# Kernel optimization log

Measured on AMD Instinct MI355X. Metric: run time of the kernel, lower is better.

The kernel has to match this reference:

```python
import jax, jax.numpy as jnp
import numpy as np

B, T, D = 2, 2048, 2048
N_HEADS, N_KV = 16, 4
HD = D // N_HEADS  # 128
ROPE_BASE = 10000.0


def _rope_tables(t, dim, base=ROPE_BASE):
    inv_freq = 1.0 / (base ** (jnp.arange(0, dim, 2, dtype=jnp.float32) / dim))
    freqs = jnp.arange(t, dtype=jnp.float32)[:, None] * inv_freq[None, :]  # (T, dim/2)
    emb = jnp.concatenate([freqs, freqs], axis=-1)  # (T, dim)
    return jnp.cos(emb), jnp.sin(emb)


def _rotate_half(x):
    x1, x2 = jnp.split(x, 2, axis=-1)
    return jnp.concatenate([-x2, x1], axis=-1)


def _apply_rope(x, cos, sin):
    # x: (B, H, T, hd); cos/sin: (T, hd)
    return x * cos[None, None] + _rotate_half(x) * sin[None, None]


def setup_inputs() -> dict:
    key = jax.random.key(0)
    ks = jax.random.split(key, 5)
    s = 0.02
    return {
        "x": jax.random.normal(ks[0], (B, T, D), jnp.float32),
        "wq": jax.random.normal(ks[1], (D, N_HEADS * HD), jnp.float32) * s,
        "wk": jax.random.normal(ks[2], (D, N_KV * HD), jnp.float32) * s,
        "wv": jax.random.normal(ks[3], (D, N_KV * HD), jnp.float32) * s,
        "wo": jax.random.normal(ks[4], (D, D), jnp.float32) * s,
    }


def reference(x, wq, wk, wv, wo):
    b, t, c = x.shape
    n_rep = N_HEADS // N_KV
    scale = 1.0 / np.sqrt(HD)

    q = (x @ wq).reshape(b, t, N_HEADS, HD).transpose(0, 2, 1, 3)  # (B,H,T,hd)
    k = (x @ wk).reshape(b, t, N_KV, HD).transpose(0, 2, 1, 3)     # (B,Hkv,T,hd)
    v = (x @ wv).reshape(b, t, N_KV, HD).transpose(0, 2, 1, 3)

    cos, sin = _rope_tables(t, HD)
    q = _apply_rope(q, cos, sin)
    k = _apply_rope(k, cos, sin)

    # repeat_kv (GQA)
    k = jnp.repeat(k, n_rep, axis=1)  # (B,H,T,hd)
    v = jnp.repeat(v, n_rep, axis=1)

    scores = jnp.einsum("bhqd,bhkd->bhqk", q, k) * scale
    causal = jnp.tril(jnp.ones((t, t), dtype=bool))
    scores = jnp.where(causal[None, None], scores, -jnp.inf)
    attn = jax.nn.softmax(scores, axis=-1)
    out = jnp.einsum("bhqk,bhkd->bhqd", attn, v)
    out = out.transpose(0, 2, 1, 3).reshape(b, t, c)
    return out @ wo
```

## Files before the change

### kernel.cpp

```cpp
#include <hip/hip_runtime.h>
#include <hip/hip_bf16.h>
#include <math.h>

#define B_   2
#define T_   2048
#define D_   2048
#define NH_  16
#define NKV_ 4
#define HD_  128
#define MROWS (B_*T_)
#define NQKV  (NH_*HD_ + 2*NKV_*HD_)

typedef __bf16 bf16_t;
typedef __bf16 bf16x8 __attribute__((ext_vector_type(8)));
typedef __bf16 bf16x4 __attribute__((ext_vector_type(4)));
typedef float  floatx4 __attribute__((ext_vector_type(4)));

__device__ __forceinline__ void async_copy16(const bf16_t* gsrc, bf16_t* ldst) {
  __builtin_amdgcn_global_load_lds(
      (const __attribute__((address_space(1))) unsigned int*)gsrc,
      (__attribute__((address_space(3))) unsigned int*)ldst, 16, 0, 0);
}

__global__ void prep_fused(const float* __restrict__ s0, const float* __restrict__ s1,
                           const float* __restrict__ s2, const float* __restrict__ s3,
                           const float* __restrict__ sx,
                           bf16_t* __restrict__ d0, bf16_t* __restrict__ d1,
                           bf16_t* __restrict__ d2, bf16_t* __restrict__ d3,
                           bf16_t* __restrict__ dx) {
  const int z = blockIdx.z;
  const int tx = threadIdx.x, ty = threadIdx.y;
  if (z == 4) {
    int i = ((blockIdx.y * 64 + blockIdx.x) * 256 + ty * 32 + tx) * 8;
    float4 a = *(const float4*)(sx + i);
    float4 b = *(const float4*)(sx + i + 4);
    bf16x8 v;
    v[0]=(bf16_t)a.x; v[1]=(bf16_t)a.y; v[2]=(bf16_t)a.z; v[3]=(bf16_t)a.w;
    v[4]=(bf16_t)b.x; v[5]=(bf16_t)b.y; v[6]=(bf16_t)b.z; v[7]=(bf16_t)b.w;
    *(bf16x8*)(dx + i) = v;
    return;
  }
  const int N = (z == 1 || z == 2) ? 512 : 2048;
  const int n0 = blockIdx.x * 32;
  if (n0 >= N) return;
  const float* src = (z == 0) ? s0 : (z == 1) ? s1 : (z == 2) ? s2 : s3;
  bf16_t*      dst = (z == 0) ? d0 : (z == 1) ? d1 : (z == 2) ? d2 : d3;
  const int K = 2048;
  __shared__ float tile[32][33];
  int k0 = blockIdx.y * 32;
#pragma unroll
  for (int r = 0; r < 4; r++)
    tile[ty + r*8][tx] = src[(size_t)(k0 + ty + r*8) * N + n0 + tx];
  __syncthreads();
#pragma unroll
  for (int r = 0; r < 4; r++)
    dst[(size_t)(n0 + ty + r*8) * K + k0 + tx] = (bf16_t)tile[tx][ty + r*8];
}

template <typename OUT_T>
__global__ __launch_bounds__(256, 3)
void gemm_bt(const bf16_t* __restrict__ A, const bf16_t* __restrict__ Bt,
             OUT_T* __restrict__ C, int M, int N, int K) {
  __shared__ __align__(16) bf16_t As[128 * 64];
  __shared__ __align__(16) bf16_t Bs[128 * 64];
  const int tid  = threadIdx.x;
  const int wave = tid >> 6, lane = tid & 63;
  const int quad = lane >> 4, l16 = lane & 15;
  const int nBlocksM = M >> 7;
  const int bm = blockIdx.x % nBlocksM, bn = blockIdx.x / nBlocksM;
  const int m0 = bm * 128, n0 = bn * 128;
  const int wm = (wave >> 1) * 64, wn = (wave & 1) * 64;

  floatx4 acc[4][4];
#pragma unroll
  for (int i = 0; i < 4; i++)
#pragma unroll
    for (int j = 0; j < 4; j++) acc[i][j] = floatx4{0.f, 0.f, 0.f, 0.f};

  for (int k0 = 0; k0 < K; k0 += 64) {
    __syncthreads();
#pragma unroll
    for (int i = 0; i < 4; i++) {
      int e = i * 256 + tid;
      int row = e >> 3, grp = e & 7;
      int gg = grp ^ (row & 7);
      async_copy16(A + (size_t)(m0 + row) * K + k0 + gg * 8, As + e * 8);
    }
#pragma unroll
    for (int i = 0; i < 4; i++) {
      int e = i * 256 + tid;
      int row = e >> 3, grp = e & 7;
      int gg = grp ^ (row & 7);
      async_copy16(Bt + (size_t)(n0 + row) * K + k0 + gg * 8, Bs + e * 8);
    }
    __syncthreads();
#pragma unroll
    for (int ks = 0; ks < 2; ks++) {
      bf16x8 af[4], bfr[4];
      int grp = ks * 4 + quad;
#pragma unroll
      for (int mi = 0; mi < 4; mi++) {
        int row = wm + mi * 16 + l16;
        af[mi] = *(const bf16x8*)(As + row * 64 + ((grp ^ (row & 7)) << 3));
      }
#pragma unroll
      for (int ni = 0; ni < 4; ni++) {
        int row = wn + ni * 16 + l16;
        bfr[ni] = *(const bf16x8*)(Bs + row * 64 + ((grp ^ (row & 7)) << 3));
      }
#pragma unroll
      for (int mi = 0; mi < 4; mi++)
#pragma unroll
        for (int ni = 0; ni < 4; ni++)
          acc[mi][ni] = __builtin_amdgcn_mfma_f32_16x16x32_bf16(af[mi], bfr[ni], acc[mi][ni], 0, 0, 0);
    }
  }
#pragma unroll
  for (int mi = 0; mi < 4; mi++) {
#pragma unroll
    for (int r = 0; r < 4; r++) {
      int row = m0 + wm + mi * 16 + quad * 4 + r;
      size_t base = (size_t)row * N + n0 + wn;
#pragma unroll
      for (int ni = 0; ni < 4; ni++)
        C[base + ni * 16 + l16] = (OUT_T)acc[mi][ni][r];
    }
  }
}

#define ROPE_BLOCKS ((MROWS * NKV_ * 64) / 256)
__global__ void kv_prep(const bf16_t* __restrict__ qkv, bf16_t* __restrict__ Kb,
                        bf16_t* __restrict__ Vt) {
  if (blockIdx.x < ROPE_BLOCKS) {
    int g = blockIdx.x * 256 + threadIdx.x;
    int j = g & 63;
    int rest = g >> 6;
    int kvh = rest & 3;
    int row = rest >> 2;
    int t = row & (T_ - 1);
    int b = row >> 11;
    const bf16_t* src = qkv + (size_t)row * NQKV + NH_ * HD_ + kvh * HD_;
    float ang = (float)t * __expf(-0.14391156816f * (float)j);
    float sn, cs;
    __sincosf(ang, &sn, &cs);
    float x0 = (float)src[j];
    float x1 = (float)src[j + 64];
    bf16_t* dst = Kb + ((size_t)(b * NKV_ + kvh) * T_ + t) * HD_;
    dst[j]      = (bf16_t)(x0 * cs - x1 * sn);
    dst[j + 64] = (bf16_t)(x1 * cs + x0 * sn);
    return;
  }
  __shared__ float tile[32][33];
  int bb = blockIdx.x - ROPE_BLOCKS;
  int bx = bb & 63, by = (bb >> 6) & 3, bz = bb >> 8;
  int t0 = bx * 32, d0 = by * 32;
  int b = bz / NKV_, kvh = bz % NKV_;
  int tx = threadIdx.x & 31, ty = threadIdx.x >> 5;
#pragma unroll
  for (int r = 0; r < 4; r++) {
    int t = t0 + ty + r * 8;
    tile[ty + r*8][tx] =
        (float)qkv[(size_t)(b * T_ + t) * NQKV + (NH_ + NKV_) * HD_ + kvh * HD_ + d0 + tx];
  }
  __syncthreads();
#pragma unroll
  for (int r = 0; r < 4; r++) {
    int d = d0 + ty + r * 8;
    int t = t0 + tx;
    int k = t & 63;
    int pos = ((((k >> 4) & 1) * 4 + ((k >> 2) & 3)) << 3) + ((k >> 5) << 2) + (k & 3);
    Vt[((size_t)(b * NKV_ + kvh) * HD_ + d) * T_ + (t & ~63) + pos] =
        (bf16_t)tile[tx][ty + r*8];
  }
}

__global__ __launch_bounds__(256, 2)
void flash_attn(const bf16_t* __restrict__ qkv, const bf16_t* __restrict__ Kb,
                const bf16_t* __restrict__ Vt, bf16_t* __restrict__ Ob) {
  __shared__ __align__(16) bf16_t Ks[2][64 * 128];
  __shared__ __align__(16) bf16_t Vs[2][128 * 64];

  const int tid = threadIdx.x;
  const int wave = tid >> 6, lane = tid & 63;
  const int quad = lane >> 4, l16 = lane & 15;
  const int bid = blockIdx.x;
  const int bh = bid & 31;
  const int qtp = bid >> 5;
  const int qt2 = (qtp < 8) ? (15 - qtp) : (qtp - 8);
  const int h = bh & 15;
  const int b = bh >> 4;
  const int kv = h >> 2;
  const int q0 = qt2 * 128;
  const int ktLast = 2 * qt2 + 1;

  const bf16_t* kbase = Kb + ((size_t)(b * NKV_ + kv) * T_) * HD_;
  const bf16_t* vbase = Vt + ((size_t)(b * NKV_ + kv) * HD_) * T_;

  auto stage = [&](int kt, int bufi) {
#pragma unroll
    for (int i = 0; i < 4; i++) {
      int e = i * 256 + tid;
      int row = e >> 4, grp = e & 15;
      int gg = grp ^ (row & 15);
      async_copy16(kbase + (size_t)(kt * 64 + row) * HD_ + gg * 8, &Ks[bufi][e * 8]);
    }
#pragma unroll
    for (int i = 0; i < 4; i++) {
      int e = i * 256 + tid;
      int row = e >> 3, grp = e & 7;
      int gg = grp ^ (row & 7);
      async_copy16(vbase + (size_t)row * T_ + kt * 64 + gg * 8, &Vs[bufi][e * 8]);
    }
  };

  stage(0, 0);

  bf16x8 qf[2][4];
#pragma unroll
  for (int g = 0; g < 2; g++) {
    const int t_row = q0 + g * 64 + wave * 16 + l16;
    const bf16_t* qptr = qkv + (size_t)(b * T_ + t_row) * NQKV + h * HD_;
    bf16x8 qraw[4];
#pragma unroll
    for (int ks = 0; ks < 4; ks++)
      qraw[ks] = *(const bf16x8*)(qptr + ks * 32 + quad * 8);
    const float scale = 0.12751651541057752f;
#pragma unroll
    for (int ks = 0; ks < 2; ks++)
#pragma unroll
      for (int j = 0; j < 8; j++) {
        int d = ks * 32 + quad * 8 + j;
        float ang = (float)t_row * __expf(-0.14391156816f * (float)d);
        float sn, cs;
        __sincosf(ang, &sn, &cs);
        float lo = (float)qraw[ks][j], hi = (float)qraw[ks + 2][j];
        qf[g][ks][j]     = (bf16_t)((lo * cs - hi * sn) * scale);
        qf[g][ks + 2][j] = (bf16_t)((hi * cs + lo * sn) * scale);
      }
  }

  floatx4 o[2][8];
#pragma unroll
  for (int g = 0; g < 2; g++)
#pragma unroll
    for (int i = 0; i < 8; i++) o[g][i] = floatx4{0.f, 0.f, 0.f, 0.f};
  float m_s[2] = {-1e30f, -1e30f}, l_s[2] = {0.f, 0.f};

  const int qlocal64 = wave * 16 + l16;

  for (int kt = 0; kt <= ktLast; kt++) {
    const int bufi = kt & 1;
    __syncthreads();
    if (kt < ktLast) stage(kt + 1, bufi ^ 1);

    floatx4 s[2][4];
#pragma unroll
    for (int g = 0; g < 2; g++)
#pragma unroll
      for (int nt = 0; nt < 4; nt++) s[g][nt] = floatx4{0.f, 0.f, 0.f, 0.f};
    __builtin_amdgcn_s_setprio(1);
#pragma unroll
    for (int ks = 0; ks < 4; ks++) {
      int grp = ks * 4 + quad;
#pragma unroll
      for (int nt = 0; nt < 4; nt++) {
        int row = nt * 16 + l16;
        bf16x8 kf = *(const bf16x8*)(&Ks[bufi][row * 128 + ((grp ^ (row & 15)) << 3)]);
        s[0][nt] = __builtin_amdgcn_mfma_f32_16x16x32_bf16(kf, qf[0][ks], s[0][nt], 0, 0, 0);
        s[1][nt] = __builtin_amdgcn_mfma_f32_16x16x32_bf16(kf, qf[1][ks], s[1][nt], 0, 0, 0);
      }
    }
    __builtin_amdgcn_s_setprio(0);

#pragma unroll
    for (int g = 0; g < 2; g++) {
      int ktd = 2 * qt2 + g;
      if (kt >= ktd) {
        int koff = (kt - ktd) * 64;
#pragma unroll
        for (int nt = 0; nt < 4; nt++)
#pragma unroll
          for (int r = 0; r < 4; r++) {
            int klocal = nt * 16 + quad * 4 + r + koff;
            if (klocal > qlocal64) s[g][nt][r] = -1e30f;
          }
      }
    }

#pragma unroll
    for (int g = 0; g < 2; g++) {
      float mx = fmaxf(fmaxf(s[g][0][0], s[g][0][1]), fmaxf(s[g][0][2], s[g][0][3]));
#pragma unroll
      for (int nt = 1; nt < 4; nt++)
        mx = fmaxf(mx, fmaxf(fmaxf(s[g][nt][0], s[g][nt][1]),
                             fmaxf(s[g][nt][2], s[g][nt][3])));
      mx = fmaxf(mx, __shfl_xor(mx, 16, 64));
      mx = fmaxf(mx, __shfl_xor(mx, 32, 64));
      if (!__all(mx <= m_s[g] + 8.0f)) {
        float mnew = fmaxf(m_s[g], mx);
        float alpha = __builtin_amdgcn_exp2f(m_s[g] - mnew);
        m_s[g] = mnew;
        l_s[g] *= alpha;
#pragma unroll
        for (int dt = 0; dt < 8; dt++) o[g][dt] *= alpha;
      }
      float sum = 0.f;
#pragma unroll
      for (int nt = 0; nt < 4; nt++)
#pragma unroll
        for (int r = 0; r < 4; r++) {
          float p = __builtin_amdgcn_exp2f(s[g][nt][r] - m_s[g]);
          s[g][nt][r] = p;
          sum += p;
        }
      sum += __shfl_xor(sum, 16, 64);
      sum += __shfl_xor(sum, 32, 64);
      l_s[g] += sum;
    }

    __builtin_amdgcn_s_setprio(1);
#pragma unroll
    for (int ks = 0; ks < 2; ks++) {
      bf16x8 pf0, pf1;
#pragma unroll
      for (int j = 0; j < 4; j++) {
        pf0[j]     = (bf16_t)s[0][ks][j];
        pf0[j + 4] = (bf16_t)s[0][ks + 2][j];
        pf1[j]     = (bf16_t)s[1][ks][j];
        pf1[j + 4] = (bf16_t)s[1][ks + 2][j];
      }
      const int G = ks * 4 + quad;
#pragma unroll
      for (int dt = 0; dt < 8; dt++) {
        int row = dt * 16 + l16;
        bf16x8 vf = *(const bf16x8*)(&Vs[bufi][row * 64 + ((G ^ (row & 7)) << 3)]);
        o[0][dt] = __builtin_amdgcn_mfma_f32_16x16x32_bf16(vf, pf0, o[0][dt], 0, 0, 0);
        o[1][dt] = __builtin_amdgcn_mfma_f32_16x16x32_bf16(vf, pf1, o[1][dt], 0, 0, 0);
      }
    }
    __builtin_amdgcn_s_setprio(0);
  }

#pragma unroll
  for (int g = 0; g < 2; g++) {
    int qg = q0 + g * 64 + wave * 16 + l16;
    float inv_l = 1.f / l_s[g];
    size_t base = ((size_t)(b * T_) + qg) * D_ + h * HD_;
#pragma unroll
    for (int dt = 0; dt < 8; dt++) {
      bf16x4 w;
#pragma unroll
      for (int r = 0; r < 4; r++) w[r] = (bf16_t)(o[g][dt][r] * inv_l);
      *(bf16x4*)(Ob + base + dt * 16 + quad * 4) = w;
    }
  }
}

extern "C" void kernel_launch(void* const* d_in, const int* in_sizes, int n_in,
                              void* d_out, int out_size, void* d_ws, size_t ws_size,
                              hipStream_t stream) {
  const float* x  = (const float*)d_in[0];
  const float* wq = (const float*)d_in[1];
  const float* wk = (const float*)d_in[2];
  const float* wv = (const float*)d_in[3];
  const float* wo = (const float*)d_in[4];
  float* out = (float*)d_out;

  bf16_t* x_bf   = (bf16_t*)d_ws;
  bf16_t* attn_o = x_bf;
  bf16_t* wqkv_t = x_bf + (size_t)MROWS * D_;
  bf16_t* wo_t   = wqkv_t + (size_t)NQKV * D_;
  bf16_t* qkv    = wo_t + (size_t)D_ * D_;
  bf16_t* Kb     = qkv + (size_t)MROWS * NQKV;
  bf16_t* Vt     = Kb + (size_t)B_ * NKV_ * T_ * HD_;

  prep_fused<<<dim3(64, 64, 5), dim3(32, 8), 0, stream>>>(
      wq, wk, wv, wo, x,
      wqkv_t, wqkv_t + (size_t)2048 * D_, wqkv_t + (size_t)2560 * D_, wo_t, x_bf);

  gemm_bt<bf16_t><<<(MROWS / 128) * (NQKV / 128), 256, 0, stream>>>(
      x_bf, wqkv_t, qkv, MROWS, NQKV, D_);

  kv_prep<<<ROPE_BLOCKS + (T_ / 32) * (HD_ / 32) * B_ * NKV_, 256, 0, stream>>>(
      qkv, Kb, Vt);

  flash_attn<<<B_ * NH_ * (T_ / 128), 256, 0, stream>>>(qkv, Kb, Vt, attn_o);

  gemm_bt<float><<<(MROWS / 128) * (D_ / 128), 256, 0, stream>>>(
      attn_o, wo_t, out, MROWS, D_, D_);
}
```

Measured before the change: 284.4 us.

## Pair opposite 64-row query tiles per block to skip redundant causal work

Each flash-attention block now handles two non-adjacent 64-row query tiles, qtB = 31-j and j, so per-block causal work is balanced. Key tiles past the shorter tile's diagonal run a single-group body that skips its MFMAs and softmax, removing fully masked compute that the adjacent-tile pairing previously did on the last tile. The cost is a templated two-variant loop body with a branch per key tile, more code size and possible register pressure, and a near-constant trip count per block.

After: 280.0 us. About the same (-1.5%).

```diff
diff --git a/kernel.cpp b/kernel.cpp
--- a/kernel.cpp
+++ b/kernel.cpp
@@ -15,6 +15,8 @@
 typedef __bf16 bf16x8 __attribute__((ext_vector_type(8)));
 typedef __bf16 bf16x4 __attribute__((ext_vector_type(4)));
 typedef float  floatx4 __attribute__((ext_vector_type(4)));
+
+template <int N> struct IC { static constexpr int v = N; };
 
 __device__ __forceinline__ void async_copy16(const bf16_t* gsrc, bf16_t* ldst) {
   __builtin_amdgcn_global_load_lds(
@@ -185,13 +187,12 @@
   const int quad = lane >> 4, l16 = lane & 15;
   const int bid = blockIdx.x;
   const int bh = bid & 31;
-  const int qtp = bid >> 5;
-  const int qt2 = (qtp < 8) ? (15 - qtp) : (qtp - 8);
+  const int jA = bid >> 5;
+  const int qtB = 31 - jA;
   const int h = bh & 15;
   const int b = bh >> 4;
   const int kv = h >> 2;
-  const int q0 = qt2 * 128;
-  const int ktLast = 2 * qt2 + 1;
+  const int ktB = qtB;
 
   const bf16_t* kbase = Kb + ((size_t)(b * NKV_ + kv) * T_) * HD_;
   const bf16_t* vbase = Vt + ((size_t)(b * NKV_ + kv) * HD_) * T_;
@@ -215,10 +216,12 @@
 
   stage(0, 0);
 
+  const int qt_g[2] = { qtB, jA };
+
   bf16x8 qf[2][4];
 #pragma unroll
   for (int g = 0; g < 2; g++) {
-    const int t_row = q0 + g * 64 + wave * 16 + l16;
+    const int t_row = qt_g[g] * 64 + wave * 16 + l16;
     const bf16_t* qptr = qkv + (size_t)(b * T_ + t_row) * NQKV + h * HD_;
     bf16x8 qraw[4];
 #pragma unroll
@@ -248,102 +251,109 @@
 
   const int qlocal64 = wave * 16 + l16;
 
-  for (int kt = 0; kt <= ktLast; kt++) {
+  for (int kt = 0; kt <= ktB; kt++) {
     const int bufi = kt & 1;
     __syncthreads();
-    if (kt < ktLast) stage(kt + 1, bufi ^ 1);
-
-    floatx4 s[2][4];
-#pragma unroll
-    for (int g = 0; g < 2; g++)
-#pragma unroll
-      for (int nt = 0; nt < 4; nt++) s[g][nt] = floatx4{0.f, 0.f, 0.f, 0.f};
-    __builtin_amdgcn_s_setprio(1);
-#pragma unroll
-    for (int ks = 0; ks < 4; ks++) {
-      int grp = ks * 4 + quad;
-#pragma unroll
-      for (int nt = 0; nt < 4; nt++) {
-        int row = nt * 16 + l16;
-        bf16x8 kf = *(const bf16x8*)(&Ks[bufi][row * 128 + ((grp ^ (row & 15)) << 3)]);
-        s[0][nt] = __builtin_amdgcn_mfma_f32_16x16x32_bf16(kf, qf[0][ks], s[0][nt], 0, 0, 0);
-        s[1][nt] = __builtin_amdgcn_mfma_f32_16x16x32_bf16(kf, qf[1][ks], s[1][nt], 0, 0, 0);
-      }
-    }
-    __builtin_amdgcn_s_setprio(0);
-
-#pragma unroll
-    for (int g = 0; g < 2; g++) {
-      int ktd = 2 * qt2 + g;
-      if (kt >= ktd) {
-        int koff = (kt - ktd) * 64;
+    if (kt < ktB) stage(kt + 1, bufi ^ 1);
+
+    auto body = [&](auto ngc) {
+      constexpr int NG = decltype(ngc)::v;
+      floatx4 s[NG][4];
+#pragma unroll
+      for (int g = 0; g < NG; g++)
+#pragma unroll
+        for (int nt = 0; nt < 4; nt++) s[g][nt] = floatx4{0.f, 0.f, 0.f, 0.f};
+      __builtin_amdgcn_s_setprio(1);
+#pragma unroll
+      for (int ks = 0; ks < 4; ks++) {
+        int grp = ks * 4 + quad;
+#pragma unroll
+        for (int nt = 0; nt < 4; nt++) {
+          int row = nt * 16 + l16;
+          bf16x8 kf = *(const bf16x8*)(&Ks[bufi][row * 128 + ((grp ^ (row & 15)) << 3)]);
+#pragma unroll
+          for (int g = 0; g < NG; g++)
+            s[g][nt] = __builtin_amdgcn_mfma_f32_16x16x32_bf16(kf, qf[g][ks], s[g][nt], 0, 0, 0);
+        }
+      }
+      __builtin_amdgcn_s_setprio(0);
+
+#pragma unroll
+      for (int g = 0; g < NG; g++) {
+        if (kt == qt_g[g]) {
+#pragma unroll
+          for (int nt = 0; nt < 4; nt++)
+#pragma unroll
+            for (int r = 0; r < 4; r++) {
+              int klocal = nt * 16 + quad * 4 + r;
+              if (klocal > qlocal64) s[g][nt][r] = -1e30f;
+            }
+        }
+      }
+
+#pragma unroll
+      for (int g = 0; g < NG; g++) {
+        float mx = fmaxf(fmaxf(s[g][0][0], s[g][0][1]), fmaxf(s[g][0][2], s[g][0][3]));
+#pragma unroll
+        for (int nt = 1; nt < 4; nt++)
+          mx = fmaxf(mx, fmaxf(fmaxf(s[g][nt][0], s[g][nt][1]),
+                               fmaxf(s[g][nt][2], s[g][nt][3])));
+        mx = fmaxf(mx, __shfl_xor(mx, 16, 64));
+        mx = fmaxf(mx, __shfl_xor(mx, 32, 64));
+        if (!__all(mx <= m_s[g] + 8.0f)) {
+          float mnew = fmaxf(m_s[g], mx);
+          float alpha = __builtin_amdgcn_exp2f(m_s[g] - mnew);
+          m_s[g] = mnew;
+          l_s[g] *= alpha;
+#pragma unroll
+          for (int dt = 0; dt < 8; dt++) o[g][dt] *= alpha;
+        }
+        float sum = 0.f;
 #pragma unroll
         for (int nt = 0; nt < 4; nt++)
 #pragma unroll
           for (int r = 0; r < 4; r++) {
-            int klocal = nt * 16 + quad * 4 + r + koff;
-            if (klocal > qlocal64) s[g][nt][r] = -1e30f;
+            float p = __builtin_amdgcn_exp2f(s[g][nt][r] - m_s[g]);
+            s[g][nt][r] = p;
+            sum += p;
           }
-      }
-    }
-
-#pragma unroll
-    for (int g = 0; g < 2; g++) {
-      float mx = fmaxf(fmaxf(s[g][0][0], s[g][0][1]), fmaxf(s[g][0][2], s[g][0][3]));
-#pragma unroll
-      for (int nt = 1; nt < 4; nt++)
-        mx = fmaxf(mx, fmaxf(fmaxf(s[g][nt][0], s[g][nt][1]),
-                             fmaxf(s[g][nt][2], s[g][nt][3])));
-      mx = fmaxf(mx, __shfl_xor(mx, 16, 64));
-      mx = fmaxf(mx, __shfl_xor(mx, 32, 64));
-      if (!__all(mx <= m_s[g] + 8.0f)) {
-        float mnew = fmaxf(m_s[g], mx);
-        float alpha = __builtin_amdgcn_exp2f(m_s[g] - mnew);
-        m_s[g] = mnew;
-        l_s[g] *= alpha;
-#pragma unroll
-        for (int dt = 0; dt < 8; dt++) o[g][dt] *= alpha;
-      }
-      float sum = 0.f;
-#pragma unroll
-      for (int nt = 0; nt < 4; nt++)
-#pragma unroll
-        for (int r = 0; r < 4; r++) {
-          float p = __builtin_amdgcn_exp2f(s[g][nt][r] - m_s[g]);
-          s[g][nt][r] = p;
-          sum += p;
+        sum += __shfl_xor(sum, 16, 64);
+        sum += __shfl_xor(sum, 32, 64);
+        l_s[g] += sum;
+      }
+
+      __builtin_amdgcn_s_setprio(1);
+#pragma unroll
+      for (int ks = 0; ks < 2; ks++) {
+        bf16x8 pf[NG];
+#pragma unroll
+        for (int g = 0; g < NG; g++)
+#pragma unroll
+          for (int j = 0; j < 4; j++) {
+            pf[g][j]     = (bf16_t)s[g][ks][j];
+            pf[g][j + 4] = (bf16_t)s[g][ks + 2][j];
+          }
+        const int G = ks * 4 + quad;
+#pragma unroll
+        for (int dt = 0; dt < 8; dt++) {
+          int row = dt * 16 + l16;
+          bf16x8 vf = *(const bf16x8*)(&Vs[bufi][row * 64 + ((G ^ (row & 7)) << 3)]);
+#pragma unroll
+          for (int g = 0; g < NG; g++)
+            o[g][dt] = __builtin_amdgcn_mfma_f32_16x16x32_bf16(vf, pf[g], o[g][dt], 0, 0, 0);
         }
-      sum += __shfl_xor(sum, 16, 64);
-      sum += __shfl_xor(sum, 32, 64);
-      l_s[g] += sum;
-    }
-
-    __builtin_amdgcn_s_setprio(1);
-#pragma unroll
-    for (int ks = 0; ks < 2; ks++) {
-      bf16x8 pf0, pf1;
-#pragma unroll
-      for (int j = 0; j < 4; j++) {
-        pf0[j]     = (bf16_t)s[0][ks][j];
-        pf0[j + 4] = (bf16_t)s[0][ks + 2][j];
-        pf1[j]     = (bf16_t)s[1][ks][j];
-        pf1[j + 4] = (bf16_t)s[1][ks + 2][j];
-      }
-      const int G = ks * 4 + quad;
-#pragma unroll
-      for (int dt = 0; dt < 8; dt++) {
-        int row = dt * 16 + l16;
-        bf16x8 vf = *(const bf16x8*)(&Vs[bufi][row * 64 + ((G ^ (row & 7)) << 3)]);
-        o[0][dt] = __builtin_amdgcn_mfma_f32_16x16x32_bf16(vf, pf0, o[0][dt], 0, 0, 0);
-        o[1][dt] = __builtin_amdgcn_mfma_f32_16x16x32_bf16(vf, pf1, o[1][dt], 0, 0, 0);
-      }
-    }
-    __builtin_amdgcn_s_setprio(0);
+      }
+      __builtin_amdgcn_s_setprio(0);
+    };
+
+    if (kt <= jA) body(IC<2>{});
+    else          body(IC<1>{});
+
   }
 
 #pragma unroll
   for (int g = 0; g < 2; g++) {
-    int qg = q0 + g * 64 + wave * 16 + l16;
+    int qg = qt_g[g] * 64 + wave * 16 + l16;
     float inv_l = 1.f / l_s[g];
     size_t base = ((size_t)(b * T_) + qg) * D_ + h * HD_;
 #pragma unroll
```
